# Kernel tuning notes

Hardware: AMD Instinct MI355X
Metric: run time of the kernel (lower is better)

Reference implementation:

```python
import jax, jax.numpy as jnp
import numpy as np

D_MODEL = 128
NHEAD = 8
HEAD_DIM = D_MODEL // NHEAD  # 16
NUM_LAYERS = 7
NUM_LABELS = 2
N_NODES = 10000
N_EDGES = 160000
NEG_SLOPE = 0.2  # GATv2Conv default negative_slope


def setup_inputs() -> dict:
    key = jax.random.key(0)
    ks = jax.random.split(key, 10)
    s = 1.0 / np.sqrt(D_MODEL)
    inp = {}
    inp["x"] = jax.random.normal(ks[0], (N_NODES, D_MODEL), dtype=jnp.float32)
    inp["edge_index"] = jax.random.randint(ks[1], (2, N_EDGES), 0, N_NODES, dtype=jnp.int64)
    inp["nchunks"] = 8  # uniform extra chunk size -> chunk = NUM_LABELS + 8 = 10
    # per-layer GATv2 params, stacked on a leading layer axis
    inp["Wl"] = jax.random.normal(ks[2], (NUM_LAYERS, D_MODEL, NHEAD * HEAD_DIM), dtype=jnp.float32) * s
    inp["bl"] = jnp.zeros((NUM_LAYERS, NHEAD * HEAD_DIM), dtype=jnp.float32)
    inp["Wr"] = jax.random.normal(ks[3], (NUM_LAYERS, D_MODEL, NHEAD * HEAD_DIM), dtype=jnp.float32) * s
    inp["br"] = jnp.zeros((NUM_LAYERS, NHEAD * HEAD_DIM), dtype=jnp.float32)
    inp["att"] = jax.random.normal(ks[4], (NUM_LAYERS, NHEAD, HEAD_DIM), dtype=jnp.float32) * s
    inp["bias"] = jnp.zeros((NUM_LAYERS, NHEAD * HEAD_DIM), dtype=jnp.float32)
    # split head: Linear(d_model, 1)
    inp["w_head"] = jax.random.normal(ks[5], (D_MODEL, 1), dtype=jnp.float32) * s
    inp["b_head"] = jnp.zeros((1,), dtype=jnp.float32)
    return inp


def _gatv2_layer(x, src, dst, Wl, bl, Wr, br, att, bias):
    # GATv2: e_ij = a^T LeakyReLU(W_l x_j + W_r x_i); alpha = segment-softmax over dst; out_i = sum alpha * W_l x_j
    N = x.shape[0]
    xl = (x @ Wl + bl).reshape(N, NHEAD, HEAD_DIM)
    xr = (x @ Wr + br).reshape(N, NHEAD, HEAD_DIM)
    z = jax.nn.leaky_relu(xl[src] + xr[dst], NEG_SLOPE)          # [E, H, D]
    e = jnp.einsum('ehd,hd->eh', z, att)                          # [E, H]
    emax = jax.ops.segment_max(e, dst, num_segments=N)            # [N, H]
    ex = jnp.exp(e - emax[dst])
    denom = jax.ops.segment_sum(ex, dst, num_segments=N)          # [N, H]
    alpha = ex / (denom[dst] + 1e-16)                             # [E, H]
    out = jax.ops.segment_sum(alpha[..., None] * xl[src], dst, num_segments=N)  # [N, H, D]
    return out.reshape(N, NHEAD * HEAD_DIM) + bias


def reference(x, edge_index, nchunks, Wl, bl, Wr, br, att, bias, w_head, b_head):
    N = x.shape[0]
    loop = jnp.arange(N, dtype=edge_index.dtype)  # GATv2Conv add_self_loops=True
    src = jnp.concatenate([edge_index[0], loop])
    dst = jnp.concatenate([edge_index[1], loop])
    for i in range(NUM_LAYERS):
        x = _gatv2_layer(x, src, dst, Wl[i], bl[i], Wr[i], br[i], att[i], bias[i])
    # uniform split of size (NUM_LABELS + nchunks); keep first NUM_LABELS rows of each chunk
    chunk = NUM_LABELS + int(nchunks)
    xs = x.reshape(-1, chunk, D_MODEL)[:, :NUM_LABELS]            # [n_chunks, num_labels, d]
    out = (xs @ w_head + b_head)[..., 0]                          # [n_chunks, num_labels]
    return out
```

## Files before the change

kernel.cpp:

```cpp
#include <hip/hip_runtime.h>
#include <math.h>

#define NT 256

typedef __attribute__((ext_vector_type(8))) short bf16x8;
typedef __attribute__((ext_vector_type(4))) float f32x4;


__device__ inline int detect_is64(const int* __restrict__ ei) {
    int is64 = 1;
#pragma unroll
    for (int k = 1; k < 16; k += 2) is64 &= (ei[k] == 0);
    return is64;
}

__global__ void count_kernel(const int* __restrict__ ei, int E, int N,
                             int* __restrict__ deg) {
    int e = blockIdx.x * blockDim.x + threadIdx.x;
    if (e >= E) return;
    int is64 = detect_is64(ei);
    long long pos = (long long)E + e;
    int d = ei[is64 ? 2 * pos : pos];
    if ((unsigned)d < (unsigned)N) atomicAdd(&deg[d], 1);
}

__global__ __launch_bounds__(256) void scan_kernel(const int* __restrict__ deg,
                                                   int* __restrict__ off,
                                                   int* __restrict__ cur, int N) {
    __shared__ int wsum[4];
    int t = threadIdx.x;
    int per = (N + 255) >> 8;
    int b0 = t * per;
    int s = 0;
    for (int k = 0; k < per; k++) {
        int idx = b0 + k;
        if (idx < N) s += deg[idx];
    }
    int lane = t & 63, w = t >> 6;
    int v = s;
#pragma unroll
    for (int o = 1; o < 64; o <<= 1) {
        int u = __shfl_up(v, o, 64);
        if (lane >= o) v += u;
    }
    if (lane == 63) wsum[w] = v;
    __syncthreads();
    if (t == 0) {
        int r = 0;
#pragma unroll
        for (int j = 0; j < 4; j++) { int xx = wsum[j]; wsum[j] = r; r += xx; }
        off[N] = r;
    }
    __syncthreads();
    int run = v - s + wsum[w];
    for (int k = 0; k < per; k++) {
        int idx = b0 + k;
        if (idx < N) {
            off[idx] = run;
            cur[idx] = run;
            run += deg[idx];
        }
    }
}

__global__ void fill_kernel(const int* __restrict__ ei, int E, int N,
                            int* __restrict__ cur, int* __restrict__ esrc) {
    int e = blockIdx.x * blockDim.x + threadIdx.x;
    if (e >= E) return;
    int is64 = detect_is64(ei);
    long long spos = e;
    long long dpos = (long long)E + e;
    int s = ei[is64 ? 2 * spos : spos];
    int d = ei[is64 ? 2 * dpos : dpos];
    if ((unsigned)d >= (unsigned)N || (unsigned)s >= (unsigned)N) return;
    int p = atomicAdd(&cur[d], 1);
    esrc[p] = s;
}


__device__ inline void cvt8(const float4& a, const float4& b, bf16x8& hi, bf16x8& lo) {
    float f[8] = {a.x, a.y, a.z, a.w, b.x, b.y, b.z, b.w};
#pragma unroll
    for (int j = 0; j < 8; j++) {
        unsigned u = __float_as_uint(f[j]);
        hi[j] = (short)(u >> 16);
        float fl = f[j] - __uint_as_float(u & 0xffff0000u);
        lo[j] = (short)(__float_as_uint(fl) >> 16);
    }
}

__global__ __launch_bounds__(512, 1) void gemm_xlxr(const float* __restrict__ x,
                                                    const float* __restrict__ Wl_,
                                                    const float* __restrict__ blv,
                                                    const float* __restrict__ Wr_,
                                                    const float* __restrict__ brv,
                                                    float* __restrict__ xl,
                                                    float* __restrict__ xr,
                                                    int N, int ntiles) {
    int t = threadIdx.x;
    int w = t >> 6, lane = t & 63, q = lane >> 4, cl = lane & 15;

    bf16x8 Bh[2][4], Bl[2][4];
    float biasv[2];
    float* outp[2];
    int colc[2];
#pragma unroll
    for (int nt = 0; nt < 2; nt++) {
        int col = w * 32 + nt * 16 + cl;
        const float* Wsrc;
        int cw;
        if (col < 128) { Wsrc = Wl_; cw = col; biasv[nt] = blv[col]; outp[nt] = xl; colc[nt] = col; }
        else           { Wsrc = Wr_; cw = col - 128; biasv[nt] = brv[cw]; outp[nt] = xr; colc[nt] = cw; }
#pragma unroll
        for (int kt = 0; kt < 4; kt++) {
            int kb = kt * 32 + q * 8;
            float4 f0, f1;
            float ftmp[8];
#pragma unroll
            for (int j = 0; j < 8; j++) ftmp[j] = Wsrc[(size_t)(kb + j) * 128 + cw];
            f0 = make_float4(ftmp[0], ftmp[1], ftmp[2], ftmp[3]);
            f1 = make_float4(ftmp[4], ftmp[5], ftmp[6], ftmp[7]);
            cvt8(f0, f1, Bh[nt][kt], Bl[nt][kt]);
        }
    }

    int rt = blockIdx.x;
    if (rt >= ntiles) return;
    float4 cur[8], nxt[8];
    {
        int row = rt * 16 + cl;
        if (row >= N) row = N - 1;
        const float* ap = x + (size_t)row * 128 + q * 8;
#pragma unroll
        for (int kt = 0; kt < 4; kt++) {
            cur[2 * kt]     = *(const float4*)(ap + kt * 32);
            cur[2 * kt + 1] = *(const float4*)(ap + kt * 32 + 4);
        }
    }

    for (; rt < ntiles; rt += gridDim.x) {
        int rn = rt + gridDim.x;
        if (rn < ntiles) {
            int row = rn * 16 + cl;
            if (row >= N) row = N - 1;
            const float* ap = x + (size_t)row * 128 + q * 8;
#pragma unroll
            for (int kt = 0; kt < 4; kt++) {
                nxt[2 * kt]     = *(const float4*)(ap + kt * 32);
                nxt[2 * kt + 1] = *(const float4*)(ap + kt * 32 + 4);
            }
        }

        bf16x8 Ah[4], Al[4];
#pragma unroll
        for (int kt = 0; kt < 4; kt++) cvt8(cur[2 * kt], cur[2 * kt + 1], Ah[kt], Al[kt]);

        f32x4 acc0 = {0.f, 0.f, 0.f, 0.f}, acc1 = {0.f, 0.f, 0.f, 0.f};
#pragma unroll
        for (int kt = 0; kt < 4; kt++) {
            acc0 = __builtin_amdgcn_mfma_f32_16x16x32_bf16(Ah[kt], Bh[0][kt], acc0, 0, 0, 0);
            acc1 = __builtin_amdgcn_mfma_f32_16x16x32_bf16(Ah[kt], Bh[1][kt], acc1, 0, 0, 0);
            acc0 = __builtin_amdgcn_mfma_f32_16x16x32_bf16(Al[kt], Bh[0][kt], acc0, 0, 0, 0);
            acc1 = __builtin_amdgcn_mfma_f32_16x16x32_bf16(Al[kt], Bh[1][kt], acc1, 0, 0, 0);
            acc0 = __builtin_amdgcn_mfma_f32_16x16x32_bf16(Ah[kt], Bl[0][kt], acc0, 0, 0, 0);
            acc1 = __builtin_amdgcn_mfma_f32_16x16x32_bf16(Ah[kt], Bl[1][kt], acc1, 0, 0, 0);
        }

#pragma unroll
        for (int nt = 0; nt < 2; nt++) {
            f32x4 a = nt ? acc1 : acc0;
#pragma unroll
            for (int r = 0; r < 4; r++) {
                int row = rt * 16 + q * 4 + r;
                if (row < N) outp[nt][(size_t)row * 128 + colc[nt]] = a[r] + biasv[nt];
            }
        }
#pragma unroll
        for (int j = 0; j < 8; j++) cur[j] = nxt[j];
    }
}


__global__ __launch_bounds__(256) void gat_agg(const float4* __restrict__ xl4,
                                               const float4* __restrict__ xr4,
                                               const int* __restrict__ off,
                                               const int* __restrict__ esrc,
                                               const float4* __restrict__ att4,
                                               const float4* __restrict__ bias4,
                                               float4* __restrict__ out4, int N) {
    int lane = threadIdx.x & 63;
    int sub = lane >> 4;
    int cl = lane & 15;
    int i = blockIdx.x * 4 + (threadIdx.x >> 6);
    if (i >= N) return;

    float4 xrA = xr4[(size_t)i * 32 + 2 * cl];
    float4 xrB = xr4[(size_t)i * 32 + 2 * cl + 1];
    float4 atA = att4[2 * cl];
    float4 atB = att4[2 * cl + 1];
    int start = off[i];
    int total = off[i + 1] - start + 1;
    int groups = (total + 3) >> 2;

    float s = 0.f;
    float4 aA = make_float4(0.f, 0.f, 0.f, 0.f);
    float4 aB = make_float4(0.f, 0.f, 0.f, 0.f);

    int k = sub;
    int src = (k < total) ? ((k == 0) ? i : esrc[start + k - 1]) : i;
    float4 vA = xl4[(size_t)src * 32 + 2 * cl];
    float4 vB = xl4[(size_t)src * 32 + 2 * cl + 1];
    int valid = (k < total);

    for (int g = 0; g < groups; g++) {
        int kn = 4 * (g + 1) + sub;
        int srcn = (kn < total) ? esrc[start + kn - 1] : i;
        float4 wA = xl4[(size_t)srcn * 32 + 2 * cl];
        float4 wB = xl4[(size_t)srcn * 32 + 2 * cl + 1];

        float z0 = vA.x + xrA.x, z1 = vA.y + xrA.y, z2 = vA.z + xrA.z, z3 = vA.w + xrA.w;
        float z4 = vB.x + xrB.x, z5 = vB.y + xrB.y, z6 = vB.z + xrB.z, z7 = vB.w + xrB.w;
        z0 = (z0 > 0.f) ? z0 : 0.2f * z0;
        z1 = (z1 > 0.f) ? z1 : 0.2f * z1;
        z2 = (z2 > 0.f) ? z2 : 0.2f * z2;
        z3 = (z3 > 0.f) ? z3 : 0.2f * z3;
        z4 = (z4 > 0.f) ? z4 : 0.2f * z4;
        z5 = (z5 > 0.f) ? z5 : 0.2f * z5;
        z6 = (z6 > 0.f) ? z6 : 0.2f * z6;
        z7 = (z7 > 0.f) ? z7 : 0.2f * z7;
        float p = z0 * atA.x + z1 * atA.y + z2 * atA.z + z3 * atA.w
                + z4 * atB.x + z5 * atB.y + z6 * atB.z + z7 * atB.w;
        p += __shfl_xor(p, 1, 64);
        p = fminf(fmaxf(p, -80.f), 80.f);
        float wgt = valid ? __expf(p) : 0.f;
        s += wgt;
        aA.x += wgt * vA.x; aA.y += wgt * vA.y; aA.z += wgt * vA.z; aA.w += wgt * vA.w;
        aB.x += wgt * vB.x; aB.y += wgt * vB.y; aB.z += wgt * vB.z; aB.w += wgt * vB.w;

        vA = wA; vB = wB;
        valid = (kn < total);
    }

#pragma unroll
    for (int o = 16; o <= 32; o <<= 1) {
        s += __shfl_xor(s, o, 64);
        aA.x += __shfl_xor(aA.x, o, 64); aA.y += __shfl_xor(aA.y, o, 64);
        aA.z += __shfl_xor(aA.z, o, 64); aA.w += __shfl_xor(aA.w, o, 64);
        aB.x += __shfl_xor(aB.x, o, 64); aB.y += __shfl_xor(aB.y, o, 64);
        aB.z += __shfl_xor(aB.z, o, 64); aB.w += __shfl_xor(aB.w, o, 64);
    }

    if (sub == 0) {
        float inv = 1.f / (s + 1e-16f);
        float4 bA = bias4[2 * cl], bB = bias4[2 * cl + 1];
        float4 oA, oB;
        oA.x = aA.x * inv + bA.x; oA.y = aA.y * inv + bA.y;
        oA.z = aA.z * inv + bA.z; oA.w = aA.w * inv + bA.w;
        oB.x = aB.x * inv + bB.x; oB.y = aB.y * inv + bB.y;
        oB.z = aB.z * inv + bB.z; oB.w = aB.w * inv + bB.w;
        out4[(size_t)i * 32 + 2 * cl] = oA;
        out4[(size_t)i * 32 + 2 * cl + 1] = oB;
    }
}


__global__ __launch_bounds__(128) void head_kernel(const float* __restrict__ x,
                                                   const float* __restrict__ w,
                                                   const float* __restrict__ bh,
                                                   const int* __restrict__ nch,
                                                   float* __restrict__ out) {
    __shared__ float r[2];
    int b = blockIdx.x, t = threadIdx.x;
    int chunk = 2 + nch[0];
    int row = (b >> 1) * chunk + (b & 1);
    float p = x[(size_t)row * 128 + t] * w[t];
#pragma unroll
    for (int o = 32; o >= 1; o >>= 1) p += __shfl_xor(p, o, 64);
    if ((t & 63) == 0) r[t >> 6] = p;
    __syncthreads();
    if (t == 0) out[b] = r[0] + r[1] + bh[0];
}


extern "C" void kernel_launch(void* const* d_in, const int* in_sizes, int n_in,
                              void* d_out, int out_size, void* d_ws, size_t ws_size,
                              hipStream_t stream) {
    const float* x0 = (const float*)d_in[0];
    const int* ei = (const int*)d_in[1];
    const int* nchunks = (const int*)d_in[2];
    const float* Wl = (const float*)d_in[3];
    const float* bl = (const float*)d_in[4];
    const float* Wr = (const float*)d_in[5];
    const float* br = (const float*)d_in[6];
    const float* att = (const float*)d_in[7];
    const float* bias = (const float*)d_in[8];
    const float* wh = (const float*)d_in[9];
    const float* bh = (const float*)d_in[10];

    const int D = 128;
    int N = in_sizes[0] / D;
    int E = in_sizes[1] / 2;
    int ntiles = (N + 15) / 16;

    size_t fN = (size_t)N * D;
    float* xl = (float*)d_ws;
    float* xr = xl + fN;
    float* xA = xr + fN;
    int* deg = (int*)(xA + fN);
    int* off = deg + N;
    int* cur = off + N + 1;
    int* esrc = cur + N;

    hipMemsetAsync(deg, 0, (size_t)N * sizeof(int), stream);
    count_kernel<<<(E + NT - 1) / NT, NT, 0, stream>>>(ei, E, N, deg);
    scan_kernel<<<1, 256, 0, stream>>>(deg, off, cur, N);
    fill_kernel<<<(E + NT - 1) / NT, NT, 0, stream>>>(ei, E, N, cur, esrc);

    int aggblocks = (N + 3) / 4;
    const float* xc = x0;
    for (int l = 0; l < 7; l++) {
        gemm_xlxr<<<256, 512, 0, stream>>>(xc, Wl + (size_t)l * D * D, bl + (size_t)l * D,
                                           Wr + (size_t)l * D * D, br + (size_t)l * D,
                                           xl, xr, N, ntiles);
        gat_agg<<<aggblocks, 256, 0, stream>>>((const float4*)xl, (const float4*)xr, off, esrc,
                                               (const float4*)(att + (size_t)l * D),
                                               (const float4*)(bias + (size_t)l * D),
                                               (float4*)xA, N);
        xc = xA;
    }

    head_kernel<<<out_size, 128, 0, stream>>>(xc, wh, bh, nchunks, (float*)d_out);
}
```

Baseline: 331.1 us.

## Fuse whole GATv2 pipeline into one cooperative persistent kernel with grid syncs

Replaces the sequence of CSR-build, per-layer GEMM, aggregation and head launches with a single cooperative kernel of 256 blocks that uses grid.sync between phases. This removes roughly seventeen kernel launches and their gaps. The aggregation loop also gets a deeper software prefetch, keeping two neighbour rows in flight, and ping-pongs between two output buffers. In exchange the aggregation now runs on a fixed grid of 2048 waves with lower occupancy than the original launch, and a fallback multi-kernel path is kept in case the cooperative launch fails.

After: 895.2 us. +170.4%, slower.

```diff
diff --git a/kernel.cpp b/kernel.cpp
--- a/kernel.cpp
+++ b/kernel.cpp
@@ -1,5 +1,8 @@
 #include <hip/hip_runtime.h>
+#include <hip/hip_cooperative_groups.h>
 #include <math.h>
+
+namespace cg = cooperative_groups;
 
 #define NT 256
 
@@ -14,8 +17,292 @@
     return is64;
 }
 
-__global__ void count_kernel(const int* __restrict__ ei, int E, int N,
-                             int* __restrict__ deg) {
+__device__ inline void cvt8(const float4& a, const float4& b, bf16x8& hi, bf16x8& lo) {
+    float f[8] = {a.x, a.y, a.z, a.w, b.x, b.y, b.z, b.w};
+#pragma unroll
+    for (int j = 0; j < 8; j++) {
+        unsigned u = __float_as_uint(f[j]);
+        hi[j] = (short)(u >> 16);
+        float fl = f[j] - __uint_as_float(u & 0xffff0000u);
+        lo[j] = (short)(__float_as_uint(fl) >> 16);
+    }
+}
+
+
+__global__ __launch_bounds__(512, 1) void gat_mega(
+    const float* __restrict__ x0, const int* __restrict__ ei, const int* __restrict__ nch,
+    const float* __restrict__ Wl, const float* __restrict__ bl,
+    const float* __restrict__ Wr, const float* __restrict__ br,
+    const float* __restrict__ att, const float* __restrict__ bias,
+    const float* __restrict__ wh, const float* __restrict__ bh,
+    float* __restrict__ xl, float* __restrict__ xr,
+    float* __restrict__ xA, float* __restrict__ xB,
+    int* __restrict__ deg, int* __restrict__ off, int* __restrict__ cur,
+    int* __restrict__ esrc, float* __restrict__ out,
+    int out_n, int N, int E, int ntiles) {
+
+    cg::grid_group grid = cg::this_grid();
+    int t = threadIdx.x;
+    int b = blockIdx.x;
+    int wave = t >> 6, lane = t & 63;
+    int gt = b * 512 + t;
+    int gw = b * 8 + wave;
+    const int GT = gridDim.x * 512;
+    const int GW = gridDim.x * 8;
+    int q = lane >> 4, cl = lane & 15;
+
+    int is64 = detect_is64(ei);
+
+    for (int i = gt; i < N; i += GT) deg[i] = 0;
+    grid.sync();
+
+    for (int e = gt; e < E; e += GT) {
+        long long pos = (long long)E + e;
+        int d = ei[is64 ? 2 * pos : pos];
+        if ((unsigned)d < (unsigned)N) atomicAdd(&deg[d], 1);
+    }
+    grid.sync();
+
+    if (b == 0) {
+        __shared__ int wsum[8];
+        int per = (N + 511) >> 9;
+        int b0 = t * per;
+        int s = 0;
+        for (int k = 0; k < per; k++) {
+            int idx = b0 + k;
+            if (idx < N) s += deg[idx];
+        }
+        int v = s;
+#pragma unroll
+        for (int o = 1; o < 64; o <<= 1) {
+            int u = __shfl_up(v, o, 64);
+            if (lane >= o) v += u;
+        }
+        if (lane == 63) wsum[wave] = v;
+        __syncthreads();
+        if (t == 0) {
+            int r = 0;
+#pragma unroll
+            for (int j = 0; j < 8; j++) { int xx = wsum[j]; wsum[j] = r; r += xx; }
+            off[N] = r;
+        }
+        __syncthreads();
+        int run = v - s + wsum[wave];
+        for (int k = 0; k < per; k++) {
+            int idx = b0 + k;
+            if (idx < N) {
+                off[idx] = run;
+                cur[idx] = run;
+                run += deg[idx];
+            }
+        }
+    }
+    grid.sync();
+
+    for (int e = gt; e < E; e += GT) {
+        long long spos = e, dpos = (long long)E + e;
+        int s = ei[is64 ? 2 * spos : spos];
+        int d = ei[is64 ? 2 * dpos : dpos];
+        if ((unsigned)d >= (unsigned)N || (unsigned)s >= (unsigned)N) continue;
+        int p = atomicAdd(&cur[d], 1);
+        esrc[p] = s;
+    }
+    grid.sync();
+
+    const float* xc = x0;
+    float* xn = xA;
+    for (int l = 0; l < 7; l++) {
+        const float* WlL = Wl + (size_t)l * 16384;
+        const float* WrL = Wr + (size_t)l * 16384;
+        const float* blL = bl + (size_t)l * 128;
+        const float* brL = br + (size_t)l * 128;
+
+        {
+            bf16x8 Bh[2][4], Blo[2][4];
+            float biasv[2];
+            float* outp[2];
+            int colc[2];
+#pragma unroll
+            for (int nt = 0; nt < 2; nt++) {
+                int col = wave * 32 + nt * 16 + cl;
+                const float* Wsrc;
+                int cw;
+                if (col < 128) { Wsrc = WlL; cw = col; biasv[nt] = blL[col]; outp[nt] = xl; colc[nt] = col; }
+                else           { Wsrc = WrL; cw = col - 128; biasv[nt] = brL[cw]; outp[nt] = xr; colc[nt] = cw; }
+#pragma unroll
+                for (int kt = 0; kt < 4; kt++) {
+                    int kb = kt * 32 + q * 8;
+                    float ftmp[8];
+#pragma unroll
+                    for (int j = 0; j < 8; j++) ftmp[j] = Wsrc[(size_t)(kb + j) * 128 + cw];
+                    float4 f0 = make_float4(ftmp[0], ftmp[1], ftmp[2], ftmp[3]);
+                    float4 f1 = make_float4(ftmp[4], ftmp[5], ftmp[6], ftmp[7]);
+                    cvt8(f0, f1, Bh[nt][kt], Blo[nt][kt]);
+                }
+            }
+
+            int rt = b;
+            if (rt < ntiles) {
+                float4 curA[8], nxt[8];
+                {
+                    int row = rt * 16 + cl;
+                    if (row >= N) row = N - 1;
+                    const float* ap = xc + (size_t)row * 128 + q * 8;
+#pragma unroll
+                    for (int kt = 0; kt < 4; kt++) {
+                        curA[2 * kt]     = *(const float4*)(ap + kt * 32);
+                        curA[2 * kt + 1] = *(const float4*)(ap + kt * 32 + 4);
+                    }
+                }
+                for (; rt < ntiles; rt += gridDim.x) {
+                    int rn = rt + gridDim.x;
+                    if (rn < ntiles) {
+                        int row = rn * 16 + cl;
+                        if (row >= N) row = N - 1;
+                        const float* ap = xc + (size_t)row * 128 + q * 8;
+#pragma unroll
+                        for (int kt = 0; kt < 4; kt++) {
+                            nxt[2 * kt]     = *(const float4*)(ap + kt * 32);
+                            nxt[2 * kt + 1] = *(const float4*)(ap + kt * 32 + 4);
+                        }
+                    }
+                    bf16x8 Ah[4], Al[4];
+#pragma unroll
+                    for (int kt = 0; kt < 4; kt++) cvt8(curA[2 * kt], curA[2 * kt + 1], Ah[kt], Al[kt]);
+
+                    f32x4 acc0 = {0.f, 0.f, 0.f, 0.f}, acc1 = {0.f, 0.f, 0.f, 0.f};
+#pragma unroll
+                    for (int kt = 0; kt < 4; kt++) {
+                        acc0 = __builtin_amdgcn_mfma_f32_16x16x32_bf16(Ah[kt], Bh[0][kt], acc0, 0, 0, 0);
+                        acc1 = __builtin_amdgcn_mfma_f32_16x16x32_bf16(Ah[kt], Bh[1][kt], acc1, 0, 0, 0);
+                        acc0 = __builtin_amdgcn_mfma_f32_16x16x32_bf16(Al[kt], Bh[0][kt], acc0, 0, 0, 0);
+                        acc1 = __builtin_amdgcn_mfma_f32_16x16x32_bf16(Al[kt], Bh[1][kt], acc1, 0, 0, 0);
+                        acc0 = __builtin_amdgcn_mfma_f32_16x16x32_bf16(Ah[kt], Blo[0][kt], acc0, 0, 0, 0);
+                        acc1 = __builtin_amdgcn_mfma_f32_16x16x32_bf16(Ah[kt], Blo[1][kt], acc1, 0, 0, 0);
+                    }
+#pragma unroll
+                    for (int nt = 0; nt < 2; nt++) {
+                        f32x4 a = nt ? acc1 : acc0;
+#pragma unroll
+                        for (int r = 0; r < 4; r++) {
+                            int row = rt * 16 + q * 4 + r;
+                            if (row < N) outp[nt][(size_t)row * 128 + colc[nt]] = a[r] + biasv[nt];
+                        }
+                    }
+#pragma unroll
+                    for (int j = 0; j < 8; j++) curA[j] = nxt[j];
+                }
+            }
+        }
+        grid.sync();
+
+        {
+            const float4* xl4 = (const float4*)xl;
+            const float4* xr4 = (const float4*)xr;
+            const float4* att4 = (const float4*)(att + (size_t)l * 128);
+            const float4* bias4 = (const float4*)(bias + (size_t)l * 128);
+            float4* out4 = (float4*)xn;
+            int sub = lane >> 4;
+
+            for (int i = gw; i < N; i += GW) {
+                float4 xrA = xr4[(size_t)i * 32 + 2 * cl];
+                float4 xrB = xr4[(size_t)i * 32 + 2 * cl + 1];
+                float4 atA = att4[2 * cl];
+                float4 atB = att4[2 * cl + 1];
+                int start = off[i];
+                int total = off[i + 1] - start + 1;
+                int groups = (total + 3) >> 2;
+
+                int k0 = sub;
+                int s0 = (k0 < total) ? ((k0 == 0) ? i : esrc[start + k0 - 1]) : i;
+                int k1 = 4 + sub;
+                int s1 = (k1 < total) ? esrc[start + k1 - 1] : i;
+                float4 v0A = xl4[(size_t)s0 * 32 + 2 * cl];
+                float4 v0B = xl4[(size_t)s0 * 32 + 2 * cl + 1];
+                int k2 = 8 + sub;
+                int s2 = (k2 < total) ? esrc[start + k2 - 1] : i;
+                float4 v1A = xl4[(size_t)s1 * 32 + 2 * cl];
+                float4 v1B = xl4[(size_t)s1 * 32 + 2 * cl + 1];
+
+                float s = 0.f;
+                float4 aA = make_float4(0.f, 0.f, 0.f, 0.f);
+                float4 aB = make_float4(0.f, 0.f, 0.f, 0.f);
+
+                for (int g = 0; g < groups; g++) {
+                    int k3 = 4 * (g + 3) + sub;
+                    int s3 = (k3 < total) ? esrc[start + k3 - 1] : i;
+                    float4 v2A = xl4[(size_t)s2 * 32 + 2 * cl];
+                    float4 v2B = xl4[(size_t)s2 * 32 + 2 * cl + 1];
+
+                    int kc = 4 * g + sub;
+                    int valid = kc < total;
+                    float z0 = v0A.x + xrA.x, z1 = v0A.y + xrA.y, z2 = v0A.z + xrA.z, z3 = v0A.w + xrA.w;
+                    float z4 = v0B.x + xrB.x, z5 = v0B.y + xrB.y, z6 = v0B.z + xrB.z, z7 = v0B.w + xrB.w;
+                    z0 = (z0 > 0.f) ? z0 : 0.2f * z0;
+                    z1 = (z1 > 0.f) ? z1 : 0.2f * z1;
+                    z2 = (z2 > 0.f) ? z2 : 0.2f * z2;
+                    z3 = (z3 > 0.f) ? z3 : 0.2f * z3;
+                    z4 = (z4 > 0.f) ? z4 : 0.2f * z4;
+                    z5 = (z5 > 0.f) ? z5 : 0.2f * z5;
+                    z6 = (z6 > 0.f) ? z6 : 0.2f * z6;
+                    z7 = (z7 > 0.f) ? z7 : 0.2f * z7;
+                    float p = z0 * atA.x + z1 * atA.y + z2 * atA.z + z3 * atA.w
+                            + z4 * atB.x + z5 * atB.y + z6 * atB.z + z7 * atB.w;
+                    p += __shfl_xor(p, 1, 64);
+                    p = fminf(fmaxf(p, -80.f), 80.f);
+                    float wgt = valid ? __expf(p) : 0.f;
+                    s += wgt;
+                    aA.x += wgt * v0A.x; aA.y += wgt * v0A.y; aA.z += wgt * v0A.z; aA.w += wgt * v0A.w;
+                    aB.x += wgt * v0B.x; aB.y += wgt * v0B.y; aB.z += wgt * v0B.z; aB.w += wgt * v0B.w;
+
+                    v0A = v1A; v0B = v1B;
+                    v1A = v2A; v1B = v2B;
+                    s2 = s3;
+                }
+
+#pragma unroll
+                for (int o = 16; o <= 32; o <<= 1) {
+                    s += __shfl_xor(s, o, 64);
+                    aA.x += __shfl_xor(aA.x, o, 64); aA.y += __shfl_xor(aA.y, o, 64);
+                    aA.z += __shfl_xor(aA.z, o, 64); aA.w += __shfl_xor(aA.w, o, 64);
+                    aB.x += __shfl_xor(aB.x, o, 64); aB.y += __shfl_xor(aB.y, o, 64);
+                    aB.z += __shfl_xor(aB.z, o, 64); aB.w += __shfl_xor(aB.w, o, 64);
+                }
+                if (sub == 0) {
+                    float inv = 1.f / (s + 1e-16f);
+                    float4 bA = bias4[2 * cl], bB = bias4[2 * cl + 1];
+                    float4 oA, oB;
+                    oA.x = aA.x * inv + bA.x; oA.y = aA.y * inv + bA.y;
+                    oA.z = aA.z * inv + bA.z; oA.w = aA.w * inv + bA.w;
+                    oB.x = aB.x * inv + bB.x; oB.y = aB.y * inv + bB.y;
+                    oB.z = aB.z * inv + bB.z; oB.w = aB.w * inv + bB.w;
+                    out4[(size_t)i * 32 + 2 * cl] = oA;
+                    out4[(size_t)i * 32 + 2 * cl + 1] = oB;
+                }
+            }
+        }
+        grid.sync();
+
+        xc = xn;
+        xn = (xn == xA) ? xB : xA;
+    }
+
+    {
+        int chunk = 2 + nch[0];
+        float2 wv = ((const float2*)wh)[lane];
+        for (int r = gw; r < out_n; r += GW) {
+            int row = (r >> 1) * chunk + (r & 1);
+            float2 xv = ((const float2*)(xc + (size_t)row * 128))[lane];
+            float p = xv.x * wv.x + xv.y * wv.y;
+#pragma unroll
+            for (int o = 32; o >= 1; o >>= 1) p += __shfl_xor(p, o, 64);
+            if (lane == 0) out[r] = p + bh[0];
+        }
+    }
+}
+
+
+__global__ void count_kernel(const int* __restrict__ ei, int E, int N, int* __restrict__ deg) {
     int e = blockIdx.x * blockDim.x + threadIdx.x;
     if (e >= E) return;
     int is64 = detect_is64(ei);
@@ -68,25 +355,12 @@
     int e = blockIdx.x * blockDim.x + threadIdx.x;
     if (e >= E) return;
     int is64 = detect_is64(ei);
-    long long spos = e;
-    long long dpos = (long long)E + e;
+    long long spos = e, dpos = (long long)E + e;
     int s = ei[is64 ? 2 * spos : spos];
     int d = ei[is64 ? 2 * dpos : dpos];
     if ((unsigned)d >= (unsigned)N || (unsigned)s >= (unsigned)N) return;
     int p = atomicAdd(&cur[d], 1);
     esrc[p] = s;
-}
-
-
-__device__ inline void cvt8(const float4& a, const float4& b, bf16x8& hi, bf16x8& lo) {
-    float f[8] = {a.x, a.y, a.z, a.w, b.x, b.y, b.z, b.w};
-#pragma unroll
-    for (int j = 0; j < 8; j++) {
-        unsigned u = __float_as_uint(f[j]);
-        hi[j] = (short)(u >> 16);
-        float fl = f[j] - __uint_as_float(u & 0xffff0000u);
-        lo[j] = (short)(__float_as_uint(fl) >> 16);
-    }
 }
 
 __global__ __launch_bounds__(512, 1) void gemm_xlxr(const float* __restrict__ x,
@@ -99,7 +373,6 @@
                                                     int N, int ntiles) {
     int t = threadIdx.x;
     int w = t >> 6, lane = t & 63, q = lane >> 4, cl = lane & 15;
-
     bf16x8 Bh[2][4], Bl[2][4];
     float biasv[2];
     float* outp[2];
@@ -114,16 +387,14 @@
 #pragma unroll
         for (int kt = 0; kt < 4; kt++) {
             int kb = kt * 32 + q * 8;
-            float4 f0, f1;
             float ftmp[8];
 #pragma unroll
             for (int j = 0; j < 8; j++) ftmp[j] = Wsrc[(size_t)(kb + j) * 128 + cw];
-            f0 = make_float4(ftmp[0], ftmp[1], ftmp[2], ftmp[3]);
-            f1 = make_float4(ftmp[4], ftmp[5], ftmp[6], ftmp[7]);
+            float4 f0 = make_float4(ftmp[0], ftmp[1], ftmp[2], ftmp[3]);
+            float4 f1 = make_float4(ftmp[4], ftmp[5], ftmp[6], ftmp[7]);
             cvt8(f0, f1, Bh[nt][kt], Bl[nt][kt]);
         }
     }
-
     int rt = blockIdx.x;
     if (rt >= ntiles) return;
     float4 cur[8], nxt[8];
@@ -137,7 +408,6 @@
             cur[2 * kt + 1] = *(const float4*)(ap + kt * 32 + 4);
         }
     }
-
     for (; rt < ntiles; rt += gridDim.x) {
         int rn = rt + gridDim.x;
         if (rn < ntiles) {
@@ -150,11 +420,9 @@
                 nxt[2 * kt + 1] = *(const float4*)(ap + kt * 32 + 4);
             }
         }
-
         bf16x8 Ah[4], Al[4];
 #pragma unroll
         for (int kt = 0; kt < 4; kt++) cvt8(cur[2 * kt], cur[2 * kt + 1], Ah[kt], Al[kt]);
-
         f32x4 acc0 = {0.f, 0.f, 0.f, 0.f}, acc1 = {0.f, 0.f, 0.f, 0.f};
 #pragma unroll
         for (int kt = 0; kt < 4; kt++) {
@@ -165,7 +433,6 @@
             acc0 = __builtin_amdgcn_mfma_f32_16x16x32_bf16(Ah[kt], Bl[0][kt], acc0, 0, 0, 0);
             acc1 = __builtin_amdgcn_mfma_f32_16x16x32_bf16(Ah[kt], Bl[1][kt], acc1, 0, 0, 0);
         }
-
 #pragma unroll
         for (int nt = 0; nt < 2; nt++) {
             f32x4 a = nt ? acc1 : acc0;
@@ -179,7 +446,6 @@
         for (int j = 0; j < 8; j++) cur[j] = nxt[j];
     }
 }
-
 
 __global__ __launch_bounds__(256) void gat_agg(const float4* __restrict__ xl4,
                                                const float4* __restrict__ xr4,
@@ -193,7 +459,6 @@
     int cl = lane & 15;
     int i = blockIdx.x * 4 + (threadIdx.x >> 6);
     if (i >= N) return;
-
     float4 xrA = xr4[(size_t)i * 32 + 2 * cl];
     float4 xrB = xr4[(size_t)i * 32 + 2 * cl + 1];
     float4 atA = att4[2 * cl];
@@ -201,23 +466,19 @@
     int start = off[i];
     int total = off[i + 1] - start + 1;
     int groups = (total + 3) >> 2;
-
     float s = 0.f;
     float4 aA = make_float4(0.f, 0.f, 0.f, 0.f);
     float4 aB = make_float4(0.f, 0.f, 0.f, 0.f);
-
     int k = sub;
     int src = (k < total) ? ((k == 0) ? i : esrc[start + k - 1]) : i;
     float4 vA = xl4[(size_t)src * 32 + 2 * cl];
     float4 vB = xl4[(size_t)src * 32 + 2 * cl + 1];
     int valid = (k < total);
-
     for (int g = 0; g < groups; g++) {
         int kn = 4 * (g + 1) + sub;
         int srcn = (kn < total) ? esrc[start + kn - 1] : i;
         float4 wA = xl4[(size_t)srcn * 32 + 2 * cl];
         float4 wB = xl4[(size_t)srcn * 32 + 2 * cl + 1];
-
         float z0 = vA.x + xrA.x, z1 = vA.y + xrA.y, z2 = vA.z + xrA.z, z3 = vA.w + xrA.w;
         float z4 = vB.x + xrB.x, z5 = vB.y + xrB.y, z6 = vB.z + xrB.z, z7 = vB.w + xrB.w;
         z0 = (z0 > 0.f) ? z0 : 0.2f * z0;
@@ -236,11 +497,9 @@
         s += wgt;
         aA.x += wgt * vA.x; aA.y += wgt * vA.y; aA.z += wgt * vA.z; aA.w += wgt * vA.w;
         aB.x += wgt * vB.x; aB.y += wgt * vB.y; aB.z += wgt * vB.z; aB.w += wgt * vB.w;
-
         vA = wA; vB = wB;
         valid = (kn < total);
     }
-
 #pragma unroll
     for (int o = 16; o <= 32; o <<= 1) {
         s += __shfl_xor(s, o, 64);
@@ -249,7 +508,6 @@
         aB.x += __shfl_xor(aB.x, o, 64); aB.y += __shfl_xor(aB.y, o, 64);
         aB.z += __shfl_xor(aB.z, o, 64); aB.w += __shfl_xor(aB.w, o, 64);
     }
-
     if (sub == 0) {
         float inv = 1.f / (s + 1e-16f);
         float4 bA = bias4[2 * cl], bB = bias4[2 * cl + 1];
@@ -262,7 +520,6 @@
         out4[(size_t)i * 32 + 2 * cl + 1] = oB;
     }
 }
-
 
 __global__ __launch_bounds__(128) void head_kernel(const float* __restrict__ x,
                                                    const float* __restrict__ w,
@@ -296,6 +553,7 @@
     const float* bias = (const float*)d_in[8];
     const float* wh = (const float*)d_in[9];
     const float* bh = (const float*)d_in[10];
+    float* outp = (float*)d_out;
 
     const int D = 128;
     int N = in_sizes[0] / D;
@@ -306,10 +564,23 @@
     float* xl = (float*)d_ws;
     float* xr = xl + fN;
     float* xA = xr + fN;
-    int* deg = (int*)(xA + fN);
+    float* xB = xA + fN;
+    int* deg = (int*)(xB + fN);
     int* off = deg + N;
     int* cur = off + N + 1;
     int* esrc = cur + N;
+
+    void* args[] = {
+        (void*)&x0, (void*)&ei, (void*)&nchunks,
+        (void*)&Wl, (void*)&bl, (void*)&Wr, (void*)&br,
+        (void*)&att, (void*)&bias, (void*)&wh, (void*)&bh,
+        (void*)&xl, (void*)&xr, (void*)&xA, (void*)&xB,
+        (void*)&deg, (void*)&off, (void*)&cur, (void*)&esrc,
+        (void*)&outp, (void*)&out_size, (void*)&N, (void*)&E, (void*)&ntiles
+    };
+    hipError_t rc = hipLaunchCooperativeKernel((void*)gat_mega, dim3(256), dim3(512),
+                                               args, 0, stream);
+    if (rc == hipSuccess) return;
 
     hipMemsetAsync(deg, 0, (size_t)N * sizeof(int), stream);
     count_kernel<<<(E + NT - 1) / NT, NT, 0, stream>>>(ei, E, N, deg);
@@ -318,6 +589,7 @@
 
     int aggblocks = (N + 3) / 4;
     const float* xc = x0;
+    float* xn = xA;
     for (int l = 0; l < 7; l++) {
         gemm_xlxr<<<256, 512, 0, stream>>>(xc, Wl + (size_t)l * D * D, bl + (size_t)l * D,
                                            Wr + (size_t)l * D * D, br + (size_t)l * D,
@@ -325,9 +597,9 @@
         gat_agg<<<aggblocks, 256, 0, stream>>>((const float4*)xl, (const float4*)xr, off, esrc,
                                                (const float4*)(att + (size_t)l * D),
                                                (const float4*)(bias + (size_t)l * D),
-                                               (float4*)xA, N);
-        xc = xA;
-    }
-
-    head_kernel<<<out_size, 128, 0, stream>>>(xc, wh, bh, nchunks, (float*)d_out);
-}
+                                               (float4*)xn, N);
+        xc = xn;
+        xn = (xn == xA) ? xB : xA;
+    }
+    head_kernel<<<out_size, 128, 0, stream>>>(xc, wh, bh, nchunks, outp);
+}
```

## Pre-split weights into bf16 fragments and deepen gather prefetch in aggregation

Applied to the files above, without the earlier changes.

A new prep kernel converts all seven layers' Wl/Wr into hi/lo bf16 MFMA fragment layout once, through a shared-memory transpose. Each GEMM block then loads ready fragments with vector loads instead of strided scalar loads followed by conversion. The aggregation kernel now prefetches neighbour rows two steps ahead instead of one, to hide gather latency, at the cost of more registers. The node-feature output also alternates between two buffers across layers.

After: 316.6 us. -4.4%, faster.

```diff
diff --git a/kernel.cpp b/kernel.cpp
--- a/kernel.cpp
+++ b/kernel.cpp
@@ -14,8 +14,26 @@
     return is64;
 }
 
-__global__ void count_kernel(const int* __restrict__ ei, int E, int N,
-                             int* __restrict__ deg) {
+__device__ inline void split1(float f, short& hi, short& lo) {
+    unsigned u = __float_as_uint(f);
+    hi = (short)(u >> 16);
+    float fl = f - __uint_as_float(u & 0xffff0000u);
+    lo = (short)(__float_as_uint(fl) >> 16);
+}
+
+__device__ inline void cvt8(const float4& a, const float4& b, bf16x8& hi, bf16x8& lo) {
+    float f[8] = {a.x, a.y, a.z, a.w, b.x, b.y, b.z, b.w};
+#pragma unroll
+    for (int j = 0; j < 8; j++) {
+        unsigned u = __float_as_uint(f[j]);
+        hi[j] = (short)(u >> 16);
+        float fl = f[j] - __uint_as_float(u & 0xffff0000u);
+        lo[j] = (short)(__float_as_uint(fl) >> 16);
+    }
+}
+
+
+__global__ void count_kernel(const int* __restrict__ ei, int E, int N, int* __restrict__ deg) {
     int e = blockIdx.x * blockDim.x + threadIdx.x;
     if (e >= E) return;
     int is64 = detect_is64(ei);
@@ -68,8 +86,7 @@
     int e = blockIdx.x * blockDim.x + threadIdx.x;
     if (e >= E) return;
     int is64 = detect_is64(ei);
-    long long spos = e;
-    long long dpos = (long long)E + e;
+    long long spos = e, dpos = (long long)E + e;
     int s = ei[is64 ? 2 * spos : spos];
     int d = ei[is64 ? 2 * dpos : dpos];
     if ((unsigned)d >= (unsigned)N || (unsigned)s >= (unsigned)N) return;
@@ -78,21 +95,42 @@
 }
 
 
-__device__ inline void cvt8(const float4& a, const float4& b, bf16x8& hi, bf16x8& lo) {
-    float f[8] = {a.x, a.y, a.z, a.w, b.x, b.y, b.z, b.w};
+__global__ __launch_bounds__(256) void prep_w(const float* __restrict__ Wl,
+                                              const float* __restrict__ Wr,
+                                              short* __restrict__ Whi,
+                                              short* __restrict__ Wlo) {
+    __shared__ float Wt[128][17];
+    int l = blockIdx.x >> 4;
+    int tile = blockIdx.x & 15;
+    int c0 = tile * 16;
+    const float* Wsrc = (c0 < 128) ? Wl + (size_t)l * 16384 : Wr + (size_t)l * 16384;
+    int cbase = (c0 < 128) ? c0 : c0 - 128;
+    int t = threadIdx.x;
+#pragma unroll
+    for (int it = 0; it < 8; it++) {
+        int idx = it * 256 + t;
+        int k = idx >> 4, c = idx & 15;
+        Wt[k][c] = Wsrc[(size_t)k * 128 + cbase + c];
+    }
+    __syncthreads();
+    int kt = t >> 6, lane = t & 63, q = (lane >> 4), cl = lane & 15;
+    bf16x8 hi, lo;
 #pragma unroll
     for (int j = 0; j < 8; j++) {
-        unsigned u = __float_as_uint(f[j]);
-        hi[j] = (short)(u >> 16);
-        float fl = f[j] - __uint_as_float(u & 0xffff0000u);
-        lo[j] = (short)(__float_as_uint(fl) >> 16);
-    }
-}
+        short h, lw;
+        split1(Wt[kt * 32 + q * 8 + j][cl], h, lw);
+        hi[j] = h; lo[j] = lw;
+    }
+    size_t off = ((((size_t)l * 16 + tile) * 4 + kt) * 64 + lane) * 8;
+    *(bf16x8*)(Whi + off) = hi;
+    *(bf16x8*)(Wlo + off) = lo;
+}
+
 
 __global__ __launch_bounds__(512, 1) void gemm_xlxr(const float* __restrict__ x,
-                                                    const float* __restrict__ Wl_,
+                                                    const short* __restrict__ WhiL,
+                                                    const short* __restrict__ WloL,
                                                     const float* __restrict__ blv,
-                                                    const float* __restrict__ Wr_,
                                                     const float* __restrict__ brv,
                                                     float* __restrict__ xl,
                                                     float* __restrict__ xr,
@@ -106,21 +144,15 @@
     int colc[2];
 #pragma unroll
     for (int nt = 0; nt < 2; nt++) {
-        int col = w * 32 + nt * 16 + cl;
-        const float* Wsrc;
-        int cw;
-        if (col < 128) { Wsrc = Wl_; cw = col; biasv[nt] = blv[col]; outp[nt] = xl; colc[nt] = col; }
-        else           { Wsrc = Wr_; cw = col - 128; biasv[nt] = brv[cw]; outp[nt] = xr; colc[nt] = cw; }
+        int tile = w * 2 + nt;
+        int col = tile * 16 + cl;
+        if (col < 128) { biasv[nt] = blv[col]; outp[nt] = xl; colc[nt] = col; }
+        else           { biasv[nt] = brv[col - 128]; outp[nt] = xr; colc[nt] = col - 128; }
 #pragma unroll
         for (int kt = 0; kt < 4; kt++) {
-            int kb = kt * 32 + q * 8;
-            float4 f0, f1;
-            float ftmp[8];
-#pragma unroll
-            for (int j = 0; j < 8; j++) ftmp[j] = Wsrc[(size_t)(kb + j) * 128 + cw];
-            f0 = make_float4(ftmp[0], ftmp[1], ftmp[2], ftmp[3]);
-            f1 = make_float4(ftmp[4], ftmp[5], ftmp[6], ftmp[7]);
-            cvt8(f0, f1, Bh[nt][kt], Bl[nt][kt]);
+            size_t off = (((size_t)tile * 4 + kt) * 64 + lane) * 8;
+            Bh[nt][kt] = *(const bf16x8*)(WhiL + off);
+            Bl[nt][kt] = *(const bf16x8*)(WloL + off);
         }
     }
 
@@ -202,24 +234,31 @@
     int total = off[i + 1] - start + 1;
     int groups = (total + 3) >> 2;
 
+    int k0 = sub;
+    int s0 = (k0 < total) ? ((k0 == 0) ? i : esrc[start + k0 - 1]) : i;
+    int k1 = 4 + sub;
+    int s1 = (k1 < total) ? esrc[start + k1 - 1] : i;
+    float4 v0A = xl4[(size_t)s0 * 32 + 2 * cl];
+    float4 v0B = xl4[(size_t)s0 * 32 + 2 * cl + 1];
+    int k2 = 8 + sub;
+    int s2 = (k2 < total) ? esrc[start + k2 - 1] : i;
+    float4 v1A = xl4[(size_t)s1 * 32 + 2 * cl];
+    float4 v1B = xl4[(size_t)s1 * 32 + 2 * cl + 1];
+
     float s = 0.f;
     float4 aA = make_float4(0.f, 0.f, 0.f, 0.f);
     float4 aB = make_float4(0.f, 0.f, 0.f, 0.f);
 
-    int k = sub;
-    int src = (k < total) ? ((k == 0) ? i : esrc[start + k - 1]) : i;
-    float4 vA = xl4[(size_t)src * 32 + 2 * cl];
-    float4 vB = xl4[(size_t)src * 32 + 2 * cl + 1];
-    int valid = (k < total);
-
     for (int g = 0; g < groups; g++) {
-        int kn = 4 * (g + 1) + sub;
-        int srcn = (kn < total) ? esrc[start + kn - 1] : i;
-        float4 wA = xl4[(size_t)srcn * 32 + 2 * cl];
-        float4 wB = xl4[(size_t)srcn * 32 + 2 * cl + 1];
-
-        float z0 = vA.x + xrA.x, z1 = vA.y + xrA.y, z2 = vA.z + xrA.z, z3 = vA.w + xrA.w;
-        float z4 = vB.x + xrB.x, z5 = vB.y + xrB.y, z6 = vB.z + xrB.z, z7 = vB.w + xrB.w;
+        int k3 = 4 * (g + 3) + sub;
+        int s3 = (k3 < total) ? esrc[start + k3 - 1] : i;
+        float4 v2A = xl4[(size_t)s2 * 32 + 2 * cl];
+        float4 v2B = xl4[(size_t)s2 * 32 + 2 * cl + 1];
+
+        int kc = 4 * g + sub;
+        int valid = kc < total;
+        float z0 = v0A.x + xrA.x, z1 = v0A.y + xrA.y, z2 = v0A.z + xrA.z, z3 = v0A.w + xrA.w;
+        float z4 = v0B.x + xrB.x, z5 = v0B.y + xrB.y, z6 = v0B.z + xrB.z, z7 = v0B.w + xrB.w;
         z0 = (z0 > 0.f) ? z0 : 0.2f * z0;
         z1 = (z1 > 0.f) ? z1 : 0.2f * z1;
         z2 = (z2 > 0.f) ? z2 : 0.2f * z2;
@@ -234,11 +273,12 @@
         p = fminf(fmaxf(p, -80.f), 80.f);
         float wgt = valid ? __expf(p) : 0.f;
         s += wgt;
-        aA.x += wgt * vA.x; aA.y += wgt * vA.y; aA.z += wgt * vA.z; aA.w += wgt * vA.w;
-        aB.x += wgt * vB.x; aB.y += wgt * vB.y; aB.z += wgt * vB.z; aB.w += wgt * vB.w;
-
-        vA = wA; vB = wB;
-        valid = (kn < total);
+        aA.x += wgt * v0A.x; aA.y += wgt * v0A.y; aA.z += wgt * v0A.z; aA.w += wgt * v0A.w;
+        aB.x += wgt * v0B.x; aB.y += wgt * v0B.y; aB.z += wgt * v0B.z; aB.w += wgt * v0B.w;
+
+        v0A = v1A; v0B = v1B;
+        v1A = v2A; v1B = v2B;
+        s2 = s3;
     }
 
 #pragma unroll
@@ -249,7 +289,6 @@
         aB.x += __shfl_xor(aB.x, o, 64); aB.y += __shfl_xor(aB.y, o, 64);
         aB.z += __shfl_xor(aB.z, o, 64); aB.w += __shfl_xor(aB.w, o, 64);
     }
-
     if (sub == 0) {
         float inv = 1.f / (s + 1e-16f);
         float4 bA = bias4[2 * cl], bB = bias4[2 * cl + 1];
@@ -303,31 +342,37 @@
     int ntiles = (N + 15) / 16;
 
     size_t fN = (size_t)N * D;
+    const size_t WFRAG = 16 * 4 * 64 * 8;
     float* xl = (float*)d_ws;
     float* xr = xl + fN;
     float* xA = xr + fN;
-    int* deg = (int*)(xA + fN);
+    float* xB = xA + fN;
+    short* Whi = (short*)(xB + fN);
+    short* Wlo = Whi + 7 * WFRAG;
+    int* deg = (int*)(Wlo + 7 * WFRAG);
     int* off = deg + N;
     int* cur = off + N + 1;
     int* esrc = cur + N;
 
     hipMemsetAsync(deg, 0, (size_t)N * sizeof(int), stream);
+    prep_w<<<112, 256, 0, stream>>>(Wl, Wr, Whi, Wlo);
     count_kernel<<<(E + NT - 1) / NT, NT, 0, stream>>>(ei, E, N, deg);
     scan_kernel<<<1, 256, 0, stream>>>(deg, off, cur, N);
     fill_kernel<<<(E + NT - 1) / NT, NT, 0, stream>>>(ei, E, N, cur, esrc);
 
     int aggblocks = (N + 3) / 4;
     const float* xc = x0;
+    float* xn = xA;
     for (int l = 0; l < 7; l++) {
-        gemm_xlxr<<<256, 512, 0, stream>>>(xc, Wl + (size_t)l * D * D, bl + (size_t)l * D,
-                                           Wr + (size_t)l * D * D, br + (size_t)l * D,
+        gemm_xlxr<<<256, 512, 0, stream>>>(xc, Whi + (size_t)l * WFRAG, Wlo + (size_t)l * WFRAG,
+                                           bl + (size_t)l * D, br + (size_t)l * D,
                                            xl, xr, N, ntiles);
         gat_agg<<<aggblocks, 256, 0, stream>>>((const float4*)xl, (const float4*)xr, off, esrc,
                                                (const float4*)(att + (size_t)l * D),
                                                (const float4*)(bias + (size_t)l * D),
-                                               (float4*)xA, N);
-        xc = xA;
-    }
-
+                                               (float4*)xn, N);
+        xc = xn;
+        xn = (xn == xA) ? xB : xA;
+    }
     head_kernel<<<out_size, 128, 0, stream>>>(xc, wh, bh, nchunks, (float*)d_out);
 }
```
